# Kernel optimization log

Hardware: AMD Instinct MI355X
Metric: run time of the kernel (lower is better)

The kernel has to match this reference:

```python
import jax, jax.numpy as jnp
import numpy as np

N, T, H, D = 32, 2048, 1024, 384

def setup_inputs() -> dict:
    key = jax.random.key(0)
    k1, k2, k3, k4, k5 = jax.random.split(key, 5)
    scale_h = 1.0 / np.sqrt(H)
    scale_d = 1.0 / np.sqrt(D)
    return {
        "gru_output": jax.random.normal(k1, (N, T, H), dtype=jnp.float32),
        "condition": jax.random.normal(k2, (N, D), dtype=jnp.float32),
        "W_h": jax.random.normal(k3, (H, H), dtype=jnp.float32) * scale_h,
        "W_c": jax.random.normal(k4, (D, H), dtype=jnp.float32) * scale_d,
        "bias": jnp.zeros((H,), dtype=jnp.float32),
        "v": jax.random.normal(k5, (H,), dtype=jnp.float32) * scale_h,
    }

def reference(gru_output, condition, W_h, W_c, bias, v):
    # h_proj: (N, T, H); c_proj: (N, 1, H)
    h_proj = jnp.einsum("nth,hk->ntk", gru_output, W_h)
    c_proj = jnp.einsum("nd,dk->nk", condition, W_c)[:, None, :]
    energy = jnp.tanh(h_proj + c_proj + bias)          # (N, T, H)
    scores = jnp.einsum("ntk,k->nt", energy, v)        # (N, T)
    weights = jax.nn.softmax(scores, axis=-1)          # (N, T)
    context = jnp.einsum("nth,nt->nh", gru_output, weights)  # (N, H)
    return context
```

## Files before the change

### kernel.cpp

```cpp
#include <hip/hip_runtime.h>
#include <hip/hip_bf16.h>

#define N_B 32
#define T_S 2048
#define H_D 1024
#define D_C 384
#define NT  (N_B * T_S)

typedef __attribute__((ext_vector_type(8))) short bf16x8;
typedef __attribute__((ext_vector_type(4))) float f32x4;

__device__ __forceinline__ ushort f2bf(float f) {
    union { float f; unsigned u; } x; x.f = f;
    unsigned u = x.u;
    unsigned r = (u + 0x7FFFu + ((u >> 16) & 1u)) >> 16;
    return (ushort)r;
}

__device__ __forceinline__ float bf2f(ushort u) {
    union { unsigned u; float f; } x; x.u = ((unsigned)u) << 16;
    return x.f;
}

__device__ __forceinline__ float fast_tanh(float x) {
    float e = __expf(2.0f * x);
    return 1.0f - 2.0f / (e + 1.0f);
}

__device__ __forceinline__ void gl2lds16(const void* g, void* l) {
    __builtin_amdgcn_global_load_lds(
        (const __attribute__((address_space(1))) void*)g,
        (__attribute__((address_space(3))) void*)l, 16, 0, 0);
}

__global__ __launch_bounds__(256) void convert_kernel(
    const float* __restrict__ g, ushort* __restrict__ gb)
{
    const size_t base = ((size_t)blockIdx.x * 256 + threadIdx.x) * 4;
    float4 v = *(const float4*)(g + base);
    ushort4 o;
    o.x = f2bf(v.x); o.y = f2bf(v.y); o.z = f2bf(v.z); o.w = f2bf(v.w);
    *(ushort4*)(gb + base) = o;
}

__global__ __launch_bounds__(256) void transpose_kernel(
    const float* __restrict__ W, ushort* __restrict__ Wt)
{
    __shared__ ushort tile[64 * 66];
    const int bx = blockIdx.x & 15;
    const int by = blockIdx.x >> 4;
    const int t = threadIdx.x;
    #pragma unroll
    for (int i = 0; i < 16; ++i) {
        int idx = t + i * 256;
        int r = idx >> 6, c = idx & 63;
        tile[r * 66 + c] = f2bf(W[(size_t)(by * 64 + r) * H_D + bx * 64 + c]);
    }
    __syncthreads();
    #pragma unroll
    for (int i = 0; i < 16; ++i) {
        int idx = t + i * 256;
        int r = idx >> 6, c = idx & 63;
        Wt[(size_t)(bx * 64 + r) * H_D + by * 64 + c] = tile[c * 66 + r];
    }
}

__global__ __launch_bounds__(256) void cproj_kernel(
    const float* __restrict__ cond, const float* __restrict__ Wc,
    const float* __restrict__ bias, float* __restrict__ cproj)
{
    const int idx = blockIdx.x * 256 + threadIdx.x;
    const int n = idx >> 10, k = idx & 1023;
    const int d0 = blockIdx.y * 96;
    float a0 = (blockIdx.y == 0) ? bias[k] : 0.f;
    float a1 = 0.f, a2 = 0.f, a3 = 0.f;
    const float* cp = cond + n * D_C;
    for (int d = d0; d < d0 + 96; d += 4) {
        a0 = fmaf(cp[d + 0], Wc[(size_t)(d + 0) * H_D + k], a0);
        a1 = fmaf(cp[d + 1], Wc[(size_t)(d + 1) * H_D + k], a1);
        a2 = fmaf(cp[d + 2], Wc[(size_t)(d + 2) * H_D + k], a2);
        a3 = fmaf(cp[d + 3], Wc[(size_t)(d + 3) * H_D + k], a3);
    }
    atomicAdd(&cproj[idx], (a0 + a1) + (a2 + a3));
}

__global__ __launch_bounds__(256) void gemm3_kernel(
    const ushort* __restrict__ Ab, const ushort* __restrict__ Wt,
    const float* __restrict__ cproj, const float* __restrict__ v,
    float* __restrict__ spart)
{
    __shared__ __align__(16) ushort As[128 * 64];
    __shared__ __align__(16) ushort Bs[128 * 64];
    __shared__ float red[2][2][4][16];
    const int id = blockIdx.x;
    const int mb = (id & 7) + ((id >> 6) << 3);
    const int kb = (id >> 3) & 7;
    const int m0 = mb * 128;
    const int nbatch = mb >> 4;
    const int t = threadIdx.x;
    const int lane = t & 63, wave = t >> 6;
    const int wm = wave & 1, wn = wave >> 1;
    const int q = lane >> 4, ln = lane & 15;
    const int x7 = ln & 7;

    const int srow = wave * 8 + (lane >> 3);
    const int koff = ((lane & 7) ^ (lane >> 3)) * 8;
    const ushort* ag = Ab + (size_t)(m0 + srow) * H_D + koff;
    const ushort* bg = Wt + (size_t)(kb * 128 + srow) * H_D + koff;

    f32x4 acc[4][4];
    #pragma unroll
    for (int i = 0; i < 4; ++i)
        #pragma unroll
        for (int j = 0; j < 4; ++j)
            acc[i][j] = (f32x4){0.f, 0.f, 0.f, 0.f};

    for (int h0 = 0; h0 < H_D; h0 += 64) {
        if (h0) __syncthreads();
        #pragma unroll
        for (int i = 0; i < 4; ++i) {
            gl2lds16(ag + h0 + i * 32 * H_D, As + i * 2048 + wave * 512);
            gl2lds16(bg + h0 + i * 32 * H_D, Bs + i * 2048 + wave * 512);
        }
        __syncthreads();
        #pragma unroll
        for (int kk = 0; kk < 2; ++kk) {
            bf16x8 a[4], b[4];
            #pragma unroll
            for (int i = 0; i < 4; ++i) {
                int row = wm * 64 + i * 16 + ln;
                a[i] = *(const bf16x8*)(&As[row * 64 + (((kk << 2) + q) ^ x7) * 8]);
            }
            #pragma unroll
            for (int j = 0; j < 4; ++j) {
                int row = wn * 64 + j * 16 + ln;
                b[j] = *(const bf16x8*)(&Bs[row * 64 + (((kk << 2) + q) ^ x7) * 8]);
            }
            #pragma unroll
            for (int i = 0; i < 4; ++i)
                #pragma unroll
                for (int j = 0; j < 4; ++j)
                    acc[i][j] = __builtin_amdgcn_mfma_f32_16x16x32_bf16(a[i], b[j], acc[i][j], 0, 0, 0);
        }
    }

    float cpv[4], vv[4];
    const float* cpn = cproj + nbatch * H_D;
    #pragma unroll
    for (int j = 0; j < 4; ++j) {
        int col = kb * 128 + wn * 64 + j * 16 + ln;
        cpv[j] = cpn[col];
        vv[j] = v[col];
    }
    #pragma unroll
    for (int i = 0; i < 4; ++i) {
        float s0 = 0.f, s1 = 0.f, s2 = 0.f, s3 = 0.f;
        #pragma unroll
        for (int j = 0; j < 4; ++j) {
            s0 += fast_tanh(acc[i][j][0] + cpv[j]) * vv[j];
            s1 += fast_tanh(acc[i][j][1] + cpv[j]) * vv[j];
            s2 += fast_tanh(acc[i][j][2] + cpv[j]) * vv[j];
            s3 += fast_tanh(acc[i][j][3] + cpv[j]) * vv[j];
        }
        #pragma unroll
        for (int off = 1; off < 16; off <<= 1) {
            s0 += __shfl_xor(s0, off);
            s1 += __shfl_xor(s1, off);
            s2 += __shfl_xor(s2, off);
            s3 += __shfl_xor(s3, off);
        }
        if (ln == 0) {
            red[wm][wn][i][q * 4 + 0] = s0;
            red[wm][wn][i][q * 4 + 1] = s1;
            red[wm][wn][i][q * 4 + 2] = s2;
            red[wm][wn][i][q * 4 + 3] = s3;
        }
    }
    __syncthreads();
    if (t < 128) {
        int wm2 = t >> 6, idx = t & 63;
        int i2 = idx >> 4, qr = idx & 15;
        float val = red[wm2][0][i2][qr] + red[wm2][1][i2][qr];
        spart[(size_t)kb * NT + m0 + wm2 * 64 + idx] = val;
    }
}

__global__ __launch_bounds__(1024) void softmax8_kernel(
    const float* __restrict__ spart, float* __restrict__ weights)
{
    const int n = blockIdx.x;
    const int t = threadIdx.x;
    __shared__ float red[1024];
    float s0 = 0.f, s1 = 0.f;
    #pragma unroll
    for (int kb = 0; kb < 8; ++kb) {
        s0 += spart[(size_t)kb * NT + n * T_S + t];
        s1 += spart[(size_t)kb * NT + n * T_S + 1024 + t];
    }
    red[t] = fmaxf(s0, s1); __syncthreads();
    for (int s = 512; s > 0; s >>= 1) {
        if (t < s) red[t] = fmaxf(red[t], red[t + s]);
        __syncthreads();
    }
    const float mx = red[0];
    __syncthreads();
    float e0 = __expf(s0 - mx), e1 = __expf(s1 - mx);
    red[t] = e0 + e1; __syncthreads();
    for (int s = 512; s > 0; s >>= 1) {
        if (t < s) red[t] += red[t + s];
        __syncthreads();
    }
    const float inv = 1.0f / red[0];
    weights[n * T_S + t] = e0 * inv;
    weights[n * T_S + 1024 + t] = e1 * inv;
}

__global__ __launch_bounds__(256) void context3_kernel(
    const ushort* __restrict__ Ab, const float* __restrict__ weights,
    float* __restrict__ cpart)
{
    const int tb = blockIdx.x;
    const int n  = blockIdx.y;
    const int t  = threadIdx.x;
    float a0 = 0.f, a1 = 0.f, a2 = 0.f, a3 = 0.f;
    const float* wp = weights + n * T_S + tb * 128;
    const ushort* gp = Ab + (size_t)(n * T_S + tb * 128) * H_D + t * 4;
    #pragma unroll 8
    for (int tt = 0; tt < 128; ++tt) {
        float w = wp[tt];
        ushort4 gv = *(const ushort4*)(gp + (size_t)tt * H_D);
        a0 = fmaf(w, bf2f(gv.x), a0);
        a1 = fmaf(w, bf2f(gv.y), a1);
        a2 = fmaf(w, bf2f(gv.z), a2);
        a3 = fmaf(w, bf2f(gv.w), a3);
    }
    *(float4*)(cpart + ((size_t)tb * N_B + n) * H_D + t * 4) =
        make_float4(a0, a1, a2, a3);
}

__global__ __launch_bounds__(256) void reduce_kernel(
    const float* __restrict__ cpart, float* __restrict__ out)
{
    const int idx = blockIdx.x * 256 + threadIdx.x;
    float s = 0.f;
    #pragma unroll
    for (int tb = 0; tb < 16; ++tb)
        s += cpart[(size_t)tb * (N_B * H_D) + idx];
    out[idx] = s;
}

extern "C" void kernel_launch(void* const* d_in, const int* in_sizes, int n_in,
                              void* d_out, int out_size, void* d_ws, size_t ws_size,
                              hipStream_t stream)
{
    const float* gru  = (const float*)d_in[0];
    const float* cond = (const float*)d_in[1];
    const float* W_h  = (const float*)d_in[2];
    const float* W_c  = (const float*)d_in[3];
    const float* bias = (const float*)d_in[4];
    const float* v    = (const float*)d_in[5];
    float* out = (float*)d_out;

    char* ws = (char*)d_ws;
    const size_t szAb    = (size_t)NT * H_D * 2;
    const size_t szWt    = (size_t)H_D * H_D * 2;
    const size_t szCproj = (size_t)N_B * H_D * 4;
    const size_t szSpart = (size_t)8 * NT * 4;

    ushort* Ab    = (ushort*)ws;
    ushort* Wt    = (ushort*)(ws + szAb);
    float* cproj  = (float*)(ws + szAb + szWt);
    float* spart  = (float*)(ws + szAb + szWt + szCproj);
    float* cpart  = spart;
    float* wts    = (float*)(ws + szAb + szWt + szCproj + szSpart);

    hipMemsetAsync(cproj, 0, szCproj, stream);
    convert_kernel<<<65536, 256, 0, stream>>>(gru, Ab);
    transpose_kernel<<<256, 256, 0, stream>>>(W_h, Wt);
    cproj_kernel<<<dim3(128, 4), 256, 0, stream>>>(cond, W_c, bias, cproj);
    gemm3_kernel<<<4096, 256, 0, stream>>>(Ab, Wt, cproj, v, spart);
    softmax8_kernel<<<N_B, 1024, 0, stream>>>(spart, wts);
    context3_kernel<<<dim3(16, N_B), 256, 0, stream>>>(Ab, wts, cpart);
    reduce_kernel<<<128, 256, 0, stream>>>(cpart, out);
}
```

Before: 561.0 us.

## Rewrite score GEMM with 256x256 tiles and 4-stage async LDS pipeline

Replaces the 128x128-tile GEMM, which did one synchronous load and barrier per K step, with a 256x256-tile, 512-thread kernel. It uses a 4-buffer software pipeline that issues global-to-LDS loads three tiles ahead, waits with explicit waitcnt, and interleaves LDS reads with MFMA under raised priority. A new XOR swizzle and a block remap for L2 locality are added. Larger tiles halve the partial-score slices, so the softmax sums 4 slices instead of 8. The costs are much higher register and LDS use per block, and correctness depends on the hand-tuned vmcnt counts.

```diff
diff --git a/kernel.cpp b/kernel.cpp
--- a/kernel.cpp
+++ b/kernel.cpp
@@ -84,76 +84,125 @@
     atomicAdd(&cproj[idx], (a0 + a1) + (a2 + a3));
 }
 
-__global__ __launch_bounds__(256) void gemm3_kernel(
+#define BKq 32
+#define TILE_U (256 * BKq)
+
+__global__ __launch_bounds__(512, 2) void gemm4_kernel(
     const ushort* __restrict__ Ab, const ushort* __restrict__ Wt,
     const float* __restrict__ cproj, const float* __restrict__ v,
     float* __restrict__ spart)
 {
-    __shared__ __align__(16) ushort As[128 * 64];
-    __shared__ __align__(16) ushort Bs[128 * 64];
-    __shared__ float red[2][2][4][16];
-    const int id = blockIdx.x;
-    const int mb = (id & 7) + ((id >> 6) << 3);
-    const int kb = (id >> 3) & 7;
-    const int m0 = mb * 128;
-    const int nbatch = mb >> 4;
+    __shared__ __align__(16) ushort As[4][TILE_U];
+    __shared__ __align__(16) ushort Bs[4][TILE_U];
+    __shared__ float red[2][4][128];
+
+    const int bid = blockIdx.x;
+    const int wg  = (bid & 7) * 128 + (bid >> 3);
+    const int mb  = wg & 255;
+    const int nb  = wg >> 8;
+    const int m0  = mb * 256;
+    const int n0  = nb * 256;
+    const int nbatch = mb >> 3;
+
     const int t = threadIdx.x;
-    const int lane = t & 63, wave = t >> 6;
-    const int wm = wave & 1, wn = wave >> 1;
-    const int q = lane >> 4, ln = lane & 15;
-    const int x7 = ln & 7;
-
-    const int srow = wave * 8 + (lane >> 3);
-    const int koff = ((lane & 7) ^ (lane >> 3)) * 8;
-    const ushort* ag = Ab + (size_t)(m0 + srow) * H_D + koff;
-    const ushort* bg = Wt + (size_t)(kb * 128 + srow) * H_D + koff;
-
-    f32x4 acc[4][4];
-    #pragma unroll
-    for (int i = 0; i < 4; ++i)
+    const int lane = t & 63;
+    const int w = t >> 6;
+    const int wm = w >> 2, wn = w & 3;
+    const int ln = lane & 15, q = lane >> 4;
+    const int csw = q ^ (ln & 3) ^ ((ln >> 2) & 3);
+
+    const int slab = w * 2;
+    const int Rl = lane >> 2;
+    const int gsw = ((lane & 3) ^ ((lane >> 2) & 3) ^ (lane >> 4)) * 8;
+
+    const ushort* aS0 = Ab + (size_t)(m0 + slab * 16 + Rl) * H_D + gsw;
+    const ushort* aS1 = aS0 + (size_t)16 * H_D;
+    const ushort* bS0 = Wt + (size_t)(n0 + slab * 16 + Rl) * H_D + gsw;
+    const ushort* bS1 = bS0 + (size_t)16 * H_D;
+    ushort* aD = (ushort*)As + slab * 512;
+    ushort* bD = (ushort*)Bs + slab * 512;
+
+    const ushort* aR = (const ushort*)As + (wm * 128 + ln) * BKq + csw * 8;
+    const ushort* bR = (const ushort*)Bs + (wn * 64  + ln) * BKq + csw * 8;
+
+    f32x4 acc[8][4];
+    #pragma unroll
+    for (int i = 0; i < 8; ++i)
         #pragma unroll
         for (int j = 0; j < 4; ++j)
             acc[i][j] = (f32x4){0.f, 0.f, 0.f, 0.f};
 
-    for (int h0 = 0; h0 < H_D; h0 += 64) {
-        if (h0) __syncthreads();
+#define ISSUE_A(kt, WB) do { const int _o = (kt) * BKq; \
+    gl2lds16(aS0 + _o, aD + (WB) * TILE_U); \
+    gl2lds16(aS1 + _o, aD + (WB) * TILE_U + 512); } while (0)
+#define ISSUE_B(kt, WB) do { const int _o = (kt) * BKq; \
+    gl2lds16(bS0 + _o, bD + (WB) * TILE_U); \
+    gl2lds16(bS1 + _o, bD + (WB) * TILE_U + 512); } while (0)
+
+#define MF(i,j,A,B) acc[i][j] = __builtin_amdgcn_mfma_f32_16x16x32_bf16(A, B, acc[i][j], 0, 0, 0)
+
+#define TILE(kt, RB, WB, WAIT, DOISS) do { \
+    asm volatile("s_waitcnt " WAIT ::: "memory"); \
+    __builtin_amdgcn_s_barrier(); \
+    __builtin_amdgcn_sched_barrier(0); \
+    const ushort* _ar = aR + (RB) * TILE_U; \
+    const ushort* _br = bR + (RB) * TILE_U; \
+    bf16x8 _b0 = *(const bf16x8*)(_br); \
+    bf16x8 _b1 = *(const bf16x8*)(_br + 512); \
+    bf16x8 _b2 = *(const bf16x8*)(_br + 1024); \
+    bf16x8 _b3 = *(const bf16x8*)(_br + 1536); \
+    bf16x8 _a0 = *(const bf16x8*)(_ar); \
+    bf16x8 _a1 = *(const bf16x8*)(_ar + 512); \
+    bf16x8 _a2 = *(const bf16x8*)(_ar + 1024); \
+    bf16x8 _a3 = *(const bf16x8*)(_ar + 1536); \
+    if (DOISS) ISSUE_A((kt) + 3, WB); \
+    __builtin_amdgcn_s_setprio(1); \
+    MF(0,0,_a0,_b0); MF(0,1,_a0,_b1); MF(0,2,_a0,_b2); MF(0,3,_a0,_b3); \
+    MF(1,0,_a1,_b0); MF(1,1,_a1,_b1); MF(1,2,_a1,_b2); MF(1,3,_a1,_b3); \
+    MF(2,0,_a2,_b0); MF(2,1,_a2,_b1); MF(2,2,_a2,_b2); MF(2,3,_a2,_b3); \
+    MF(3,0,_a3,_b0); MF(3,1,_a3,_b1); MF(3,2,_a3,_b2); MF(3,3,_a3,_b3); \
+    __builtin_amdgcn_s_setprio(0); \
+    bf16x8 _a4 = *(const bf16x8*)(_ar + 2048); \
+    bf16x8 _a5 = *(const bf16x8*)(_ar + 2560); \
+    bf16x8 _a6 = *(const bf16x8*)(_ar + 3072); \
+    bf16x8 _a7 = *(const bf16x8*)(_ar + 3584); \
+    if (DOISS) ISSUE_B((kt) + 3, WB); \
+    __builtin_amdgcn_s_setprio(1); \
+    MF(4,0,_a4,_b0); MF(4,1,_a4,_b1); MF(4,2,_a4,_b2); MF(4,3,_a4,_b3); \
+    MF(5,0,_a5,_b0); MF(5,1,_a5,_b1); MF(5,2,_a5,_b2); MF(5,3,_a5,_b3); \
+    MF(6,0,_a6,_b0); MF(6,1,_a6,_b1); MF(6,2,_a6,_b2); MF(6,3,_a6,_b3); \
+    MF(7,0,_a7,_b0); MF(7,1,_a7,_b1); MF(7,2,_a7,_b2); MF(7,3,_a7,_b3); \
+    __builtin_amdgcn_s_setprio(0); \
+} while (0)
+
+    ISSUE_A(0, 0); ISSUE_B(0, 0);
+    ISSUE_A(1, 1); ISSUE_B(1, 1);
+    ISSUE_A(2, 2); ISSUE_B(2, 2);
+
+    #pragma unroll 1
+    for (int kt = 0; kt < 28; kt += 4) {
+        TILE(kt + 0, 0, 3, "vmcnt(8) lgkmcnt(0)", true);
+        TILE(kt + 1, 1, 0, "vmcnt(8) lgkmcnt(0)", true);
+        TILE(kt + 2, 2, 1, "vmcnt(8) lgkmcnt(0)", true);
+        TILE(kt + 3, 3, 2, "vmcnt(8) lgkmcnt(0)", true);
+    }
+    TILE(28, 0, 3, "vmcnt(8) lgkmcnt(0)", true);
+    TILE(29, 1, 0, "vmcnt(8) lgkmcnt(0)", false);
+    TILE(30, 2, 0, "vmcnt(4) lgkmcnt(0)", false);
+    TILE(31, 3, 0, "vmcnt(0) lgkmcnt(0)", false);
+
+    float cpv[4], vv[4];
+    {
+        const float* cpn = cproj + (size_t)nbatch * H_D;
         #pragma unroll
-        for (int i = 0; i < 4; ++i) {
-            gl2lds16(ag + h0 + i * 32 * H_D, As + i * 2048 + wave * 512);
-            gl2lds16(bg + h0 + i * 32 * H_D, Bs + i * 2048 + wave * 512);
+        for (int j = 0; j < 4; ++j) {
+            int col = n0 + wn * 64 + j * 16 + ln;
+            cpv[j] = cpn[col];
+            vv[j]  = v[col];
         }
-        __syncthreads();
-        #pragma unroll
-        for (int kk = 0; kk < 2; ++kk) {
-            bf16x8 a[4], b[4];
-            #pragma unroll
-            for (int i = 0; i < 4; ++i) {
-                int row = wm * 64 + i * 16 + ln;
-                a[i] = *(const bf16x8*)(&As[row * 64 + (((kk << 2) + q) ^ x7) * 8]);
-            }
-            #pragma unroll
-            for (int j = 0; j < 4; ++j) {
-                int row = wn * 64 + j * 16 + ln;
-                b[j] = *(const bf16x8*)(&Bs[row * 64 + (((kk << 2) + q) ^ x7) * 8]);
-            }
-            #pragma unroll
-            for (int i = 0; i < 4; ++i)
-                #pragma unroll
-                for (int j = 0; j < 4; ++j)
-                    acc[i][j] = __builtin_amdgcn_mfma_f32_16x16x32_bf16(a[i], b[j], acc[i][j], 0, 0, 0);
-        }
-    }
-
-    float cpv[4], vv[4];
-    const float* cpn = cproj + nbatch * H_D;
-    #pragma unroll
-    for (int j = 0; j < 4; ++j) {
-        int col = kb * 128 + wn * 64 + j * 16 + ln;
-        cpv[j] = cpn[col];
-        vv[j] = v[col];
-    }
-    #pragma unroll
-    for (int i = 0; i < 4; ++i) {
+    }
+    #pragma unroll
+    for (int i = 0; i < 8; ++i) {
         float s0 = 0.f, s1 = 0.f, s2 = 0.f, s3 = 0.f;
         #pragma unroll
         for (int j = 0; j < 4; ++j) {
@@ -170,18 +219,18 @@
             s3 += __shfl_xor(s3, off);
         }
         if (ln == 0) {
-            red[wm][wn][i][q * 4 + 0] = s0;
-            red[wm][wn][i][q * 4 + 1] = s1;
-            red[wm][wn][i][q * 4 + 2] = s2;
-            red[wm][wn][i][q * 4 + 3] = s3;
+            red[wm][wn][i * 16 + q * 4 + 0] = s0;
+            red[wm][wn][i * 16 + q * 4 + 1] = s1;
+            red[wm][wn][i * 16 + q * 4 + 2] = s2;
+            red[wm][wn][i * 16 + q * 4 + 3] = s3;
         }
     }
     __syncthreads();
-    if (t < 128) {
-        int wm2 = t >> 6, idx = t & 63;
-        int i2 = idx >> 4, qr = idx & 15;
-        float val = red[wm2][0][i2][qr] + red[wm2][1][i2][qr];
-        spart[(size_t)kb * NT + m0 + wm2 * 64 + idx] = val;
+    if (t < 256) {
+        const int wm2 = t >> 7, row = t & 127;
+        float val = red[wm2][0][row] + red[wm2][1][row]
+                  + red[wm2][2][row] + red[wm2][3][row];
+        spart[(size_t)nb * NT + m0 + wm2 * 128 + row] = val;
     }
 }
 
@@ -193,7 +242,7 @@
     __shared__ float red[1024];
     float s0 = 0.f, s1 = 0.f;
     #pragma unroll
-    for (int kb = 0; kb < 8; ++kb) {
+    for (int kb = 0; kb < 4; ++kb) {
         s0 += spart[(size_t)kb * NT + n * T_S + t];
         s1 += spart[(size_t)kb * NT + n * T_S + 1024 + t];
     }
@@ -278,7 +327,7 @@
     convert_kernel<<<65536, 256, 0, stream>>>(gru, Ab);
     transpose_kernel<<<256, 256, 0, stream>>>(W_h, Wt);
     cproj_kernel<<<dim3(128, 4), 256, 0, stream>>>(cond, W_c, bias, cproj);
-    gemm3_kernel<<<4096, 256, 0, stream>>>(Ab, Wt, cproj, v, spart);
+    gemm4_kernel<<<1024, 512, 0, stream>>>(Ab, Wt, cproj, v, spart);
     softmax8_kernel<<<N_B, 1024, 0, stream>>>(spart, wts);
     context3_kernel<<<dim3(16, N_B), 256, 0, stream>>>(Ab, wts, cpart);
     reduce_kernel<<<128, 256, 0, stream>>>(cpart, out);
```

After: 581.0 us. 3.6% more time.
